# Kernel tuning notes

Hardware: AMD Instinct MI355X
Metric: run time of the kernel (lower is better)

The kernel has to match this reference:

```python
import jax, jax.numpy as jnp
import numpy as np

N_GROUPS = 40
MAX_DISPARITY = 48


def _groupwise(l, r, n_groups):
    # l, r: (N, C, H, W') -> (N, G, H, W') mean over channels within each group
    n, c, h, w = l.shape
    return (l * r).reshape(n, n_groups, c // n_groups, h, w).mean(axis=2)


def setup_inputs() -> dict:
    key = jax.random.key(0)
    k1, k2 = jax.random.split(key)
    left = jax.random.normal(k1, (4, 320, 80, 160), dtype=jnp.float32)
    right = jax.random.normal(k2, (4, 320, 80, 160), dtype=jnp.float32)
    return {"left": left, "right": right}


def reference(left, right):
    # Output: (N, n_groups, H, W, max_disparity) cost volume.
    n, c, h, w = left.shape
    slices = []
    for d in range(MAX_DISPARITY):  # static, small, structurally distinct shifts
        if d == 0:
            cost = _groupwise(left, right, N_GROUPS)
        else:
            cost = _groupwise(left[:, :, :, d:], right[:, :, :, : w - d], N_GROUPS)
            cost = jnp.pad(cost, ((0, 0), (0, 0), (0, 0), (d, 0)))  # zeros where w < d
        slices.append(cost)
    return jnp.stack(slices, axis=-1)
```

## Files before the change

### kernel.cpp

```cpp
#include <hip/hip_runtime.h>

typedef float f4 __attribute__((ext_vector_type(4)));

constexpr int N_  = 4;
constexpr int C_  = 320;
constexpr int H_  = 80;
constexpr int W_  = 160;
constexpr int G_  = 40;
constexpr int CPG = 8;
constexpr int D_  = 48;
constexpr int PAD = 48;
constexpr int RW  = PAD + W_;
constexpr int TILES = (W_ / 4) * (D_ / 4);

__global__ __launch_bounds__(256) void gw_cost_kernel(const float* __restrict__ Lg,
                                                      const float* __restrict__ Rg,
                                                      float* __restrict__ out) {
    __shared__ float Ls[CPG][W_];
    __shared__ float Rs[CPG][RW];

    const int blk = blockIdx.x;
    const int h = blk % H_;
    const int g = (blk / H_) % G_;
    const int n = blk / (H_ * G_);

    const int tid = threadIdx.x;

    for (int i = tid; i < CPG * (W_ / 4); i += 256) {
        const int ci = i / (W_ / 4);
        const int w4 = i % (W_ / 4);
        const size_t gb = ((size_t)(n * C_ + g * CPG + ci) * H_ + h) * W_;
        *(f4*)&Ls[ci][w4 * 4]       = *(const f4*)(Lg + gb + w4 * 4);
        *(f4*)&Rs[ci][PAD + w4 * 4] = *(const f4*)(Rg + gb + w4 * 4);
    }
    for (int i = tid; i < CPG * (PAD / 4); i += 256) {
        const int ci = i / (PAD / 4);
        const int p4 = i % (PAD / 4);
        *(f4*)&Rs[ci][p4 * 4] = (f4)(0.0f);
    }
    __syncthreads();

    const size_t ob = (size_t)blk * (W_ * D_);

    for (int t = tid; t < TILES; t += 256) {
        const int tw = t / (D_ / 4);
        const int td = t % (D_ / 4);
        const int w0 = tw * 4;
        const int d0 = td * 4;
        const int r0 = w0 - d0 + PAD;

        f4 acc0 = (f4)(0.0f);
        f4 acc1 = (f4)(0.0f);
        f4 acc2 = (f4)(0.0f);
        f4 acc3 = (f4)(0.0f);

        #pragma unroll
        for (int c = 0; c < CPG; ++c) {
            const f4 lv = *(const f4*)&Ls[c][w0];
            const f4 ra = *(const f4*)&Rs[c][r0 - 4];
            const f4 rb = *(const f4*)&Rs[c][r0];
            float rr[8];
            #pragma unroll
            for (int k = 0; k < 4; ++k) { rr[k] = ra[k]; rr[k + 4] = rb[k]; }
            #pragma unroll
            for (int j = 0; j < 4; ++j) {
                acc0[j] += lv[0] * rr[4 + 0 - j];
                acc1[j] += lv[1] * rr[4 + 1 - j];
                acc2[j] += lv[2] * rr[4 + 2 - j];
                acc3[j] += lv[3] * rr[4 + 3 - j];
            }
        }

        float* op = out + ob + (size_t)w0 * D_ + d0;
        *(f4*)(op + 0 * D_) = acc0 * 0.125f;
        *(f4*)(op + 1 * D_) = acc1 * 0.125f;
        *(f4*)(op + 2 * D_) = acc2 * 0.125f;
        *(f4*)(op + 3 * D_) = acc3 * 0.125f;
    }
}

extern "C" void kernel_launch(void* const* d_in, const int* in_sizes, int n_in,
                              void* d_out, int out_size, void* d_ws, size_t ws_size,
                              hipStream_t stream) {
    const float* Lg = (const float*)d_in[0];
    const float* Rg = (const float*)d_in[1];
    float* out = (float*)d_out;

    const int nblocks = N_ * G_ * H_;
    gw_cost_kernel<<<dim3(nblocks), dim3(256), 0, stream>>>(Lg, Rg, out);
}
```

Measured before the change: 108.7 us.

## Process two rows per block and widen disparity tile to eight

Each block now loads and computes two image rows for a channel group, halving the grid size, and each thread computes a 4x8 (width x disparity) tile instead of 4x4. This amortizes block launch and shared-memory staging overhead and increases register reuse of loaded right-image values. It raises per-thread register use and keeps the same number of tile passes per block.

```diff
diff --git a/kernel.cpp b/kernel.cpp
--- a/kernel.cpp
+++ b/kernel.cpp
@@ -11,71 +11,75 @@
 constexpr int D_  = 48;
 constexpr int PAD = 48;
 constexpr int RW  = PAD + W_;
-constexpr int TILES = (W_ / 4) * (D_ / 4);
+constexpr int H2  = 2;
 
 __global__ __launch_bounds__(256) void gw_cost_kernel(const float* __restrict__ Lg,
                                                       const float* __restrict__ Rg,
                                                       float* __restrict__ out) {
-    __shared__ float Ls[CPG][W_];
-    __shared__ float Rs[CPG][RW];
+    __shared__ float Ls[CPG * H2 * W_];
+    __shared__ float Rs[CPG * H2 * RW];
 
     const int blk = blockIdx.x;
-    const int h = blk % H_;
-    const int g = (blk / H_) % G_;
-    const int n = blk / (H_ * G_);
+    const int h2 = blk % (H_ / H2);
+    const int g  = (blk / (H_ / H2)) % G_;
+    const int n  = blk / ((H_ / H2) * G_);
+    const int h0 = h2 * H2;
 
     const int tid = threadIdx.x;
 
-    for (int i = tid; i < CPG * (W_ / 4); i += 256) {
-        const int ci = i / (W_ / 4);
-        const int w4 = i % (W_ / 4);
-        const size_t gb = ((size_t)(n * C_ + g * CPG + ci) * H_ + h) * W_;
-        *(f4*)&Ls[ci][w4 * 4]       = *(const f4*)(Lg + gb + w4 * 4);
-        *(f4*)&Rs[ci][PAD + w4 * 4] = *(const f4*)(Rg + gb + w4 * 4);
+    for (int i = tid; i < CPG * (H2 * W_ / 4); i += 256) {
+        const int c   = i / 80;
+        const int rem = i % 80;
+        const size_t gb = ((size_t)(n * C_ + g * CPG + c) * H_ + h0) * W_ + rem * 4;
+        *(f4*)&Ls[c * 320 + rem * 4] = *(const f4*)(Lg + gb);
+        const int hh = rem / 40, w4 = rem % 40;
+        *(f4*)&Rs[c * 416 + hh * 208 + PAD + w4 * 4] = *(const f4*)(Rg + gb);
     }
-    for (int i = tid; i < CPG * (PAD / 4); i += 256) {
-        const int ci = i / (PAD / 4);
-        const int p4 = i % (PAD / 4);
-        *(f4*)&Rs[ci][p4 * 4] = (f4)(0.0f);
+    for (int i = tid; i < CPG * H2 * (PAD / 4); i += 256) {
+        const int c   = i / 24;
+        const int rem = i % 24;
+        const int hh = rem / 12, p4 = rem % 12;
+        *(f4*)&Rs[c * 416 + hh * 208 + p4 * 4] = (f4)(0.0f);
     }
     __syncthreads();
 
-    const size_t ob = (size_t)blk * (W_ * D_);
-
-    for (int t = tid; t < TILES; t += 256) {
-        const int tw = t / (D_ / 4);
-        const int td = t % (D_ / 4);
+    for (int t = tid; t < H2 * 240; t += 256) {
+        const int hh  = t / 240;
+        const int rem = t % 240;
+        const int tw = rem / 6;
+        const int td = rem % 6;
         const int w0 = tw * 4;
-        const int d0 = td * 4;
+        const int d0 = td * 8;
         const int r0 = w0 - d0 + PAD;
 
-        f4 acc0 = (f4)(0.0f);
-        f4 acc1 = (f4)(0.0f);
-        f4 acc2 = (f4)(0.0f);
-        f4 acc3 = (f4)(0.0f);
+        f4 acc[4][2] = {};
 
         #pragma unroll
         for (int c = 0; c < CPG; ++c) {
-            const f4 lv = *(const f4*)&Ls[c][w0];
-            const f4 ra = *(const f4*)&Rs[c][r0 - 4];
-            const f4 rb = *(const f4*)&Rs[c][r0];
-            float rr[8];
+            const f4 lv = *(const f4*)&Ls[c * 320 + hh * 160 + w0];
+            const float* rp = &Rs[c * 416 + hh * 208 + (r0 - 8)];
+            const f4 ra = *(const f4*)(rp);
+            const f4 rb = *(const f4*)(rp + 4);
+            const f4 rc = *(const f4*)(rp + 8);
+            float r[12];
             #pragma unroll
-            for (int k = 0; k < 4; ++k) { rr[k] = ra[k]; rr[k + 4] = rb[k]; }
+            for (int k = 0; k < 4; ++k) { r[k] = ra[k]; r[4 + k] = rb[k]; r[8 + k] = rc[k]; }
             #pragma unroll
-            for (int j = 0; j < 4; ++j) {
-                acc0[j] += lv[0] * rr[4 + 0 - j];
-                acc1[j] += lv[1] * rr[4 + 1 - j];
-                acc2[j] += lv[2] * rr[4 + 2 - j];
-                acc3[j] += lv[3] * rr[4 + 3 - j];
+            for (int i = 0; i < 4; ++i) {
+                #pragma unroll
+                for (int j = 0; j < 8; ++j) {
+                    acc[i][j >> 2][j & 3] += lv[i] * r[8 + i - j];
+                }
             }
         }
 
+        const size_t ob = ((size_t)((n * G_ + g) * H_ + h0 + hh)) * (W_ * D_);
         float* op = out + ob + (size_t)w0 * D_ + d0;
-        *(f4*)(op + 0 * D_) = acc0 * 0.125f;
-        *(f4*)(op + 1 * D_) = acc1 * 0.125f;
-        *(f4*)(op + 2 * D_) = acc2 * 0.125f;
-        *(f4*)(op + 3 * D_) = acc3 * 0.125f;
+        #pragma unroll
+        for (int i = 0; i < 4; ++i) {
+            *(f4*)(op + i * D_)     = acc[i][0] * 0.125f;
+            *(f4*)(op + i * D_ + 4) = acc[i][1] * 0.125f;
+        }
     }
 }
 
@@ -86,6 +90,6 @@
     const float* Rg = (const float*)d_in[1];
     float* out = (float*)d_out;
 
-    const int nblocks = N_ * G_ * H_;
+    const int nblocks = N_ * G_ * (H_ / H2);
     gw_cost_kernel<<<dim3(nblocks), dim3(256), 0, stream>>>(Lg, Rg, out);
 }
```

Result: slower. 111.7 us (+2.7%).

## Use persistent blocks with register-staged prefetch of next row

Applied to the files above, without the earlier changes.

Replaces the one-block-per-row grid with a persistent grid of 2048 blocks that loop over rows. While computing the current row from LDS, each thread loads the next row's left and right data into registers, then writes it to LDS between two barriers. The goal is to hide global load latency behind compute and output stores. The cost is extra barriers, more register pressure, and a smaller grid that may limit latency hiding for the output-store-bound workload.

```diff
diff --git a/kernel.cpp b/kernel.cpp
--- a/kernel.cpp
+++ b/kernel.cpp
@@ -12,70 +12,113 @@
 constexpr int PAD = 48;
 constexpr int RW  = PAD + W_;
 constexpr int TILES = (W_ / 4) * (D_ / 4);
+constexpr int ROWS  = N_ * G_ * H_;
+constexpr int NBLK  = 2048;
+constexpr int NF4   = 2 * CPG * (W_ / 4);
+
+__device__ __forceinline__ void stage_load(const float* __restrict__ Lg,
+                                           const float* __restrict__ Rg,
+                                           int r, f4 (&rb)[3], int tid) {
+    const int h = r % H_;
+    const int g = (r / H_) % G_;
+    const int n = r / (H_ * G_);
+    const size_t base = (size_t)(n * C_ + g * CPG) * (H_ * W_) + (size_t)h * W_;
+    #pragma unroll
+    for (int k = 0; k < 3; ++k) {
+        const int i = tid + k * 256;
+        if (i < NF4) {
+            const int j = (i < 320) ? i : (i - 320);
+            const int c = j / 40, w4 = j % 40;
+            const float* src = ((i < 320) ? Lg : Rg) + base + (size_t)c * (H_ * W_) + w4 * 4;
+            rb[k] = *(const f4*)src;
+        }
+    }
+}
+
+__device__ __forceinline__ void stage_write(float* __restrict__ Ls,
+                                            float* __restrict__ Rs,
+                                            const f4 (&rb)[3], int tid) {
+    #pragma unroll
+    for (int k = 0; k < 3; ++k) {
+        const int i = tid + k * 256;
+        if (i < NF4) {
+            if (i < 320) {
+                const int c = i / 40, w4 = i % 40;
+                *(f4*)&Ls[c * W_ + w4 * 4] = rb[k];
+            } else {
+                const int j = i - 320;
+                const int c = j / 40, w4 = j % 40;
+                *(f4*)&Rs[c * RW + PAD + w4 * 4] = rb[k];
+            }
+        }
+    }
+}
 
 __global__ __launch_bounds__(256) void gw_cost_kernel(const float* __restrict__ Lg,
                                                       const float* __restrict__ Rg,
                                                       float* __restrict__ out) {
-    __shared__ float Ls[CPG][W_];
-    __shared__ float Rs[CPG][RW];
-
-    const int blk = blockIdx.x;
-    const int h = blk % H_;
-    const int g = (blk / H_) % G_;
-    const int n = blk / (H_ * G_);
+    __shared__ float Ls[CPG * W_];
+    __shared__ float Rs[CPG * RW];
 
     const int tid = threadIdx.x;
+    const int bid = blockIdx.x;
 
-    for (int i = tid; i < CPG * (W_ / 4); i += 256) {
-        const int ci = i / (W_ / 4);
-        const int w4 = i % (W_ / 4);
-        const size_t gb = ((size_t)(n * C_ + g * CPG + ci) * H_ + h) * W_;
-        *(f4*)&Ls[ci][w4 * 4]       = *(const f4*)(Lg + gb + w4 * 4);
-        *(f4*)&Rs[ci][PAD + w4 * 4] = *(const f4*)(Rg + gb + w4 * 4);
+    for (int i = tid; i < CPG * (PAD / 4); i += 256) {
+        const int c = i / 12, p4 = i % 12;
+        *(f4*)&Rs[c * RW + p4 * 4] = (f4)(0.0f);
     }
-    for (int i = tid; i < CPG * (PAD / 4); i += 256) {
-        const int ci = i / (PAD / 4);
-        const int p4 = i % (PAD / 4);
-        *(f4*)&Rs[ci][p4 * 4] = (f4)(0.0f);
-    }
+
+    f4 rbuf[3];
+
+    stage_load(Lg, Rg, bid, rbuf, tid);
+    stage_write(Ls, Rs, rbuf, tid);
     __syncthreads();
 
-    const size_t ob = (size_t)blk * (W_ * D_);
+    for (int r = bid; r < ROWS; r += NBLK) {
+        const int rn = r + NBLK;
+        const bool more = (rn < ROWS);
 
-    for (int t = tid; t < TILES; t += 256) {
-        const int tw = t / (D_ / 4);
-        const int td = t % (D_ / 4);
-        const int w0 = tw * 4;
-        const int d0 = td * 4;
-        const int r0 = w0 - d0 + PAD;
+        if (more) stage_load(Lg, Rg, rn, rbuf, tid);
 
-        f4 acc0 = (f4)(0.0f);
-        f4 acc1 = (f4)(0.0f);
-        f4 acc2 = (f4)(0.0f);
-        f4 acc3 = (f4)(0.0f);
+        for (int t = tid; t < TILES; t += 256) {
+            const int tw = t / 12;
+            const int td = t % 12;
+            const int w0 = tw * 4;
+            const int d0 = td * 4;
+            const int r0 = w0 - d0 + PAD;
 
-        #pragma unroll
-        for (int c = 0; c < CPG; ++c) {
-            const f4 lv = *(const f4*)&Ls[c][w0];
-            const f4 ra = *(const f4*)&Rs[c][r0 - 4];
-            const f4 rb = *(const f4*)&Rs[c][r0];
-            float rr[8];
+            f4 acc0 = (f4)(0.0f), acc1 = (f4)(0.0f), acc2 = (f4)(0.0f), acc3 = (f4)(0.0f);
+
             #pragma unroll
-            for (int k = 0; k < 4; ++k) { rr[k] = ra[k]; rr[k + 4] = rb[k]; }
-            #pragma unroll
-            for (int j = 0; j < 4; ++j) {
-                acc0[j] += lv[0] * rr[4 + 0 - j];
-                acc1[j] += lv[1] * rr[4 + 1 - j];
-                acc2[j] += lv[2] * rr[4 + 2 - j];
-                acc3[j] += lv[3] * rr[4 + 3 - j];
+            for (int c = 0; c < CPG; ++c) {
+                const f4 lv = *(const f4*)&Ls[c * W_ + w0];
+                const float* rp = &Rs[c * RW + (r0 - 4)];
+                const f4 ra = *(const f4*)(rp);
+                const f4 rb2 = *(const f4*)(rp + 4);
+                float rr[8];
+                #pragma unroll
+                for (int k = 0; k < 4; ++k) { rr[k] = ra[k]; rr[4 + k] = rb2[k]; }
+                #pragma unroll
+                for (int j = 0; j < 4; ++j) {
+                    acc0[j] += lv[0] * rr[4 + 0 - j];
+                    acc1[j] += lv[1] * rr[4 + 1 - j];
+                    acc2[j] += lv[2] * rr[4 + 2 - j];
+                    acc3[j] += lv[3] * rr[4 + 3 - j];
+                }
             }
+
+            float* op = out + (size_t)r * (W_ * D_) + (size_t)w0 * D_ + d0;
+            *(f4*)(op + 0 * D_) = acc0 * 0.125f;
+            *(f4*)(op + 1 * D_) = acc1 * 0.125f;
+            *(f4*)(op + 2 * D_) = acc2 * 0.125f;
+            *(f4*)(op + 3 * D_) = acc3 * 0.125f;
         }
 
-        float* op = out + ob + (size_t)w0 * D_ + d0;
-        *(f4*)(op + 0 * D_) = acc0 * 0.125f;
-        *(f4*)(op + 1 * D_) = acc1 * 0.125f;
-        *(f4*)(op + 2 * D_) = acc2 * 0.125f;
-        *(f4*)(op + 3 * D_) = acc3 * 0.125f;
+        if (more) {
+            __syncthreads();
+            stage_write(Ls, Rs, rbuf, tid);
+            __syncthreads();
+        }
     }
 }
 
@@ -86,6 +129,5 @@
     const float* Rg = (const float*)d_in[1];
     float* out = (float*)d_out;
 
-    const int nblocks = N_ * G_ * H_;
-    gw_cost_kernel<<<dim3(nblocks), dim3(256), 0, stream>>>(Lg, Rg, out);
+    gw_cost_kernel<<<dim3(NBLK), dim3(256), 0, stream>>>(Lg, Rg, out);
 }
```

Result: slower. 120.9 us (+11.2%).
